# Kernel tuning notes

Measured on AMD Instinct MI355X. Metric: run time of the kernel, lower is better.

The kernel has to match this reference:

```python
import jax, jax.numpy as jnp
import numpy as np

N_STFT = 513
N_BARKS = 128
SAMPLE_RATE = 16000
F_MIN = 0.0
F_MAX = 8000.0
MAX_ITER = 30
TOL_LOSS = 1e-5
TOL_CHANGE = 1e-8
LR = 0.1
MOMENTUM = 0.9
BATCH = 4
TIME = 512


def _hz_to_bark(f):
    # traunmuller scale
    b = 26.81 * f / (1960.0 + f) - 0.53
    b = jnp.where(b < 2.0, b + 0.15 * (2.0 - b), b)
    b = jnp.where(b > 20.1, b + 0.22 * (b - 20.1), b)
    return b


def _bark_to_hz(b):
    b = jnp.where(b < 2.0, (b - 0.3) / 0.85, b)
    b = jnp.where(b > 20.1, (b + 4.422) / 1.22, b)
    return 1960.0 * (b + 0.53) / (26.28 - b)


def barkscale_fbanks():
    all_freqs = jnp.linspace(0.0, float(SAMPLE_RATE // 2), N_STFT)
    b_min = _hz_to_bark(jnp.float32(F_MIN))
    b_max = _hz_to_bark(jnp.float32(F_MAX))
    b_pts = jnp.linspace(b_min, b_max, N_BARKS + 2)
    f_pts = _bark_to_hz(b_pts)
    f_diff = f_pts[1:] - f_pts[:-1]                  # (n_barks+1,)
    slopes = f_pts[None, :] - all_freqs[:, None]     # (freq, n_barks+2)
    down = -slopes[:, :-2] / f_diff[:-1]
    up = slopes[:, 2:] / f_diff[1:]
    return jnp.maximum(0.0, jnp.minimum(down, up))   # (freq, n_barks)


def setup_inputs() -> dict:
    key = jax.random.key(0)
    k1, k2 = jax.random.split(key)
    barkspec = jax.random.uniform(k1, (BATCH, N_BARKS, TIME), dtype=jnp.float32)
    fb = barkscale_fbanks().astype(jnp.float32)                 # (freq, n_barks)
    spec_init = jax.random.uniform(k2, (BATCH, TIME, N_STFT), dtype=jnp.float32)
    return {"barkspec": barkspec, "fb": fb, "spec_init": spec_init}


def reference(barkspec, fb, spec_init):
    B, K, T = barkspec.shape
    m = jnp.swapaxes(barkspec, -1, -2)          # (B, T, n_barks)
    inv_n = 1.0 / (B * T)

    def step(carry, _):
        spec, buf, prev_loss, done = carry
        diff = m - jnp.einsum('btf,fk->btk', spec, fb)          # (B, T, K)
        loss = (diff * diff).sum(-1).mean()
        # closed-form grad of mean_{b,t} sum_k diff^2 wrt spec
        grad = (-2.0 * inv_n) * jnp.einsum('btk,fk->btf', diff, fb)
        # torch SGD with momentum, no dampening/nesterov
        buf_n = MOMENTUM * buf + grad
        spec_n = jnp.maximum(spec - LR * buf_n, 0.0)            # clamp(min=0)
        stop = (loss < TOL_LOSS) | (jnp.abs(prev_loss - loss) < TOL_CHANGE)
        spec = jnp.where(done, spec, spec_n)
        buf = jnp.where(done, buf, buf_n)
        prev = jnp.where(done, prev_loss, loss)
        return (spec, buf, prev, done | stop), None

    init = (spec_init, jnp.zeros_like(spec_init), jnp.float32(jnp.inf),
            jnp.array(False))
    (spec, _, _, _), _ = jax.lax.scan(step, init, None, length=MAX_ITER)
    return jnp.swapaxes(spec, -1, -2)           # (B, freq, T)
```

## Files before the change

### kernel.cpp

```cpp
#include <hip/hip_runtime.h>


#define NSTFT 513
#define NBARK 128
#define BATCH 4
#define TIME  512
#define MAXIT 30
#define NROWS (BATCH*TIME)
#define SA 6
#define SB 20

#define WS_L_OFF   16
#define WS_FT_OFF  256
#define WS_HA_OFF  8464
#define WS_HB_OFF  8976
#define WS_WT_OFF  9488
#define WS_BP_OFF  22848

__global__ __launch_bounds__(64) void setup_taps(const float* __restrict__ fb,
                                                 char* __restrict__ ws) {
    const int f = blockIdx.x, lane = threadIdx.x;
    const float2 v = ((const float2*)(fb + (size_t)f * NBARK))[lane];
    unsigned long long mx = __ballot(v.x > 0.f);
    unsigned long long my = __ballot(v.y > 0.f);
    int kx = mx ? 2 * (__ffsll(mx) - 1)     : 999;
    int ky = my ? 2 * (__ffsll(my) - 1) + 1 : 999;
    int k1 = min(kx, ky);
    float w1 = 0.f, w2 = 0.f;
    if (k1 < NBARK) {
        float sx = __shfl(v.x, k1 >> 1);
        float sy = __shfl(v.y, k1 >> 1);
        w1 = (k1 & 1) ? sy : sx;
        const int k2 = k1 + 1;
        if (k2 < NBARK) {
            float tx = __shfl(v.x, k2 >> 1);
            float ty = __shfl(v.y, k2 >> 1);
            w2 = (k2 & 1) ? ty : tx;
        }
    } else {
        k1 = (f < 256) ? 0 : 127;
    }
    if (lane == 0) {
        float4 e;
        e.x = __int_as_float(k1); e.y = w1;
        e.z = 0.f;                e.w = w2;
        ((float4*)(ws + WS_FT_OFF))[f] = e;
    }
}

__global__ __launch_bounds__(64) void setup_lanes(char* __restrict__ ws) {
    const int c = blockIdx.x, lane = threadIdx.x;
    const float4* ftab = (const float4*)(ws + WS_FT_OFF);
    int fmin = 0x7fffffff, fmax = -1;
#pragma unroll
    for (int s = 0; s < 9; ++s) {
        int f = lane + 64*s;
        if (f < NSTFT) {
            float4 e = ftab[f];
            if (__float_as_int(e.x) == c) { fmin = min(fmin, f); fmax = max(fmax, f); }
        }
    }
#pragma unroll
    for (int m = 32; m; m >>= 1) {
        fmin = min(fmin, __shfl_xor(fmin, m));
        fmax = max(fmax, __shfl_xor(fmax, m));
    }
    int cnt = (fmax >= 0) ? (fmax - fmin + 1) : 0;
    if (fmax < 0) fmin = 0;
    const int cap  = (c < 64) ? SA : SB;
    const int base = (c < 64) ? 0  : SA;
    const int lf   = (c < 64) ? c  : 127 - c;
    cnt = min(cnt, cap);
    if (lane == 0)
        ((int2*)(ws + (c < 64 ? WS_HA_OFF : WS_HB_OFF)))[lf] =
            make_int2(fmin, cnt);
    if (lane < cap) {
        float2 wv = make_float2(0.f, 0.f);
        if (lane < cnt) {
            float4 e = ftab[fmin + lane];
            wv = make_float2(e.y, e.w);
        }
        ((float2*)(ws + WS_WT_OFF))[(base + lane)*64 + lf] = wv;
    }
}

__global__ __launch_bounds__(64, 2) void
iter_kernel(const float* __restrict__ barkspec,
            const float* __restrict__ spec_init,
            float* __restrict__ out,
            char* __restrict__ ws, int mode)
{
    const int lane = threadIdx.x;

    int niter = MAXIT;
    if (mode) {
        const float* losses = (const float*)(ws + WS_L_OFF);
        float prev = __builtin_inff();
        int S = MAXIT;
        for (int i = 0; i < MAXIT; ++i) {
            float l = losses[i];
            if (l < 1e-5f || fabsf(prev - l) < 1e-8f) { S = i + 1; break; }
            prev = l;
        }
        if (S >= MAXIT) return;
        niter = S;
    }

    const int r     = blockIdx.x;
    const int batch = r >> 9;
    const int t     = r & (TIME - 1);

    const int2 hA = ((const int2*)(ws + WS_HA_OFF))[lane];
    const int2 hB = ((const int2*)(ws + WS_HB_OFF))[lane];
    const float2* wt = (const float2*)(ws + WS_WT_OFF);
    const float* spg = spec_init + ((size_t)batch*TIME + t)*NSTFT;

    float w1A[SA], w2A[SA], spA[SA], bfA[SA];
    float w1B[SB], w2B[SB], spB[SB], bfB[SB];
#pragma unroll
    for (int i = 0; i < SA; ++i) {
        float2 v = wt[i*64 + lane];
        w1A[i] = v.x; w2A[i] = v.y;
        spA[i] = (i < hA.y) ? spg[hA.x + i] : 0.f;
        bfA[i] = 0.f;
    }
#pragma unroll
    for (int i = 0; i < SB; ++i) {
        float2 v = wt[(SA + i)*64 + lane];
        w1B[i] = v.x; w2B[i] = v.y;
        spB[i] = (i < hB.y) ? spg[hB.x + i] : 0.f;
        bfB[i] = 0.f;
    }

    const float* bs = barkspec + (size_t)batch*NBARK*TIME + t;
    const float m0 = bs[(size_t)lane*TIME];
    const float m1 = bs[(size_t)(127 - lane)*TIME];

    float* bpL = (float*)(ws + WS_BP_OFF) + (size_t)r*64 + lane;
    const float GC = -2.0f / (float)NROWS;

    for (int it = 0; it < niter; ++it) {
        float sBA = 0.f, sBB0 = 0.f, sBB1 = 0.f;
#pragma unroll
        for (int i = 0; i < SA; ++i) sBA = fmaf(spA[i], w2A[i], sBA);
#pragma unroll
        for (int i = 0; i < SB/2; ++i) sBB0 = fmaf(spB[i], w2B[i], sBB0);
#pragma unroll
        for (int i = SB/2; i < SB; ++i) sBB1 = fmaf(spB[i], w2B[i], sBB1);
        const float sBB = sBB0 + sBB1;
        float cAin = __shfl_up(sBA, 1);
        float cBin = __shfl_down(sBB, 1);

        float sAA = 0.f, sAB0 = 0.f, sAB1 = 0.f;
#pragma unroll
        for (int i = 0; i < SA; ++i) sAA = fmaf(spA[i], w1A[i], sAA);
#pragma unroll
        for (int i = 0; i < SB/2; ++i) sAB0 = fmaf(spB[i], w1B[i], sAB0);
#pragma unroll
        for (int i = SB/2; i < SB; ++i) sAB1 = fmaf(spB[i], w1B[i], sAB1);
        const float sAB = sAB0 + sAB1;

        if (lane == 0)  cAin = 0.f;
        if (lane == 63) cBin = sBA;
        const float d0 = m0 - (sAA + cAin);
        const float d1 = m1 - (sAB + cBin);

        if (!mode) { bpL[0] = fmaf(d0, d0, d1*d1); bpL += NROWS*64; }

        float dAn = __shfl_down(d0, 1);
        float dBn = __shfl_up(d1, 1);
        const float g0 = GC * d0, g1 = GC * d1;
#pragma unroll
        for (int i = 0; i < SA; ++i) bfA[i] *= 0.9f;
#pragma unroll
        for (int i = 0; i < SB; ++i) bfB[i] *= 0.9f;
        if (lane == 63) dAn = d1;
        const float gA = GC * dAn, gB = GC * dBn;
#pragma unroll
        for (int i = 0; i < SA; ++i) {
            float g = fmaf(g0, w1A[i], gA * w2A[i]);
            bfA[i] += g;
            float v = fmaf(-0.1f, bfA[i], spA[i]);
            spA[i] = v < 0.f ? 0.f : v;
        }
#pragma unroll
        for (int i = 0; i < SB; ++i) {
            float g = fmaf(g1, w1B[i], gB * w2B[i]);
            bfB[i] += g;
            float v = fmaf(-0.1f, bfB[i], spB[i]);
            spB[i] = v < 0.f ? 0.f : v;
        }
    }

    float* og = out + ((size_t)batch*NSTFT)*TIME + t;
#pragma unroll
    for (int i = 0; i < SA; ++i)
        if (i < hA.y) og[(size_t)(hA.x + i)*TIME] = spA[i];
#pragma unroll
    for (int i = 0; i < SB; ++i)
        if (i < hB.y) og[(size_t)(hB.x + i)*TIME] = spB[i];
}

__global__ __launch_bounds__(1024) void scan_reduce(char* __restrict__ ws) {
    __shared__ float wsum[16];
    const int it = blockIdx.x, tid = threadIdx.x;
    const int wave = tid >> 6, lane = tid & 63;
    const float4* b4 = (const float4*)((const float*)(ws + WS_BP_OFF)
                                       + (size_t)it*NROWS*64);
    float s = 0.f;
#pragma unroll
    for (int j = 0; j < 32; ++j) {
        float4 v = b4[tid + j*1024];
        s += (v.x + v.y) + (v.z + v.w);
    }
#pragma unroll
    for (int m = 32; m; m >>= 1) s += __shfl_xor(s, m);
    if (lane == 0) wsum[wave] = s;
    __syncthreads();
    if (wave == 0) {
        float v = (lane < 16) ? wsum[lane] : 0.f;
#pragma unroll
        for (int m = 8; m; m >>= 1) v += __shfl_xor(v, m);
        if (lane == 0)
            ((float*)(ws + WS_L_OFF))[it] = v * (1.0f/(float)NROWS);
    }
}

extern "C" void kernel_launch(void* const* d_in, const int* in_sizes, int n_in,
                              void* d_out, int out_size, void* d_ws, size_t ws_size,
                              hipStream_t stream)
{
    const float* barkspec  = (const float*)d_in[0];
    const float* fb        = (const float*)d_in[1];
    const float* spec_init = (const float*)d_in[2];
    float* out = (float*)d_out;
    char* ws = (char*)d_ws;

    setup_taps <<<NSTFT, 64, 0, stream>>>(fb, ws);
    setup_lanes<<<NBARK, 64, 0, stream>>>(ws);
    iter_kernel<<<NROWS, 64, 0, stream>>>(barkspec, spec_init, out, ws, 0);
    scan_reduce<<<MAXIT, 1024, 0, stream>>>(ws);
    iter_kernel<<<NROWS, 64, 0, stream>>>(barkspec, spec_init, out, ws, 1);
}
```

Measured before the change: 109.3 us.

## Process two time rows per wavefront and restructure shuffle dependency chain

Each 64-lane block now handles two adjacent time rows, sharing the per-lane filter weights in registers and halving the grid. The per-iteration schedule computes both dot products before any cross-lane shuffle, so all four shuffles run together and the d values are rebuilt algebraically. This is meant to give more independent work per wave to hide shuffle and FMA latency and to amortise weight loads. In exchange it doubles the state registers per thread, relaxes launch bounds to one block, and leaves fewer waves resident.

```diff
diff --git a/kernel.cpp b/kernel.cpp
--- a/kernel.cpp
+++ b/kernel.cpp
@@ -84,7 +84,7 @@
     }
 }
 
-__global__ __launch_bounds__(64, 2) void
+__global__ __launch_bounds__(64, 1) void
 iter_kernel(const float* __restrict__ barkspec,
             const float* __restrict__ spec_init,
             float* __restrict__ out,
@@ -106,99 +106,138 @@
         niter = S;
     }
 
-    const int r     = blockIdx.x;
-    const int batch = r >> 9;
-    const int t     = r & (TIME - 1);
+    const int r0    = blockIdx.x * 2;
+    const int batch = r0 >> 9;
+    const int t0    = r0 & (TIME - 1);
 
     const int2 hA = ((const int2*)(ws + WS_HA_OFF))[lane];
     const int2 hB = ((const int2*)(ws + WS_HB_OFF))[lane];
     const float2* wt = (const float2*)(ws + WS_WT_OFF);
-    const float* spg = spec_init + ((size_t)batch*TIME + t)*NSTFT;
-
-    float w1A[SA], w2A[SA], spA[SA], bfA[SA];
-    float w1B[SB], w2B[SB], spB[SB], bfB[SB];
+    const float* spg = spec_init + ((size_t)batch*TIME + t0)*NSTFT;
+
+    float w1A[SA], w2A[SA], w1B[SB], w2B[SB];
+    float spA[2][SA], bfA[2][SA], spB[2][SB], bfB[2][SB];
 #pragma unroll
     for (int i = 0; i < SA; ++i) {
         float2 v = wt[i*64 + lane];
         w1A[i] = v.x; w2A[i] = v.y;
-        spA[i] = (i < hA.y) ? spg[hA.x + i] : 0.f;
-        bfA[i] = 0.f;
+        spA[0][i] = (i < hA.y) ? spg[hA.x + i] : 0.f;
+        spA[1][i] = (i < hA.y) ? spg[NSTFT + hA.x + i] : 0.f;
+        bfA[0][i] = 0.f; bfA[1][i] = 0.f;
     }
 #pragma unroll
     for (int i = 0; i < SB; ++i) {
         float2 v = wt[(SA + i)*64 + lane];
         w1B[i] = v.x; w2B[i] = v.y;
-        spB[i] = (i < hB.y) ? spg[hB.x + i] : 0.f;
-        bfB[i] = 0.f;
-    }
-
-    const float* bs = barkspec + (size_t)batch*NBARK*TIME + t;
-    const float m0 = bs[(size_t)lane*TIME];
-    const float m1 = bs[(size_t)(127 - lane)*TIME];
-
-    float* bpL = (float*)(ws + WS_BP_OFF) + (size_t)r*64 + lane;
+        spB[0][i] = (i < hB.y) ? spg[hB.x + i] : 0.f;
+        spB[1][i] = (i < hB.y) ? spg[NSTFT + hB.x + i] : 0.f;
+        bfB[0][i] = 0.f; bfB[1][i] = 0.f;
+    }
+
+    const float* bs = barkspec + (size_t)batch*NBARK*TIME + t0;
+    const float m0[2] = { bs[(size_t)lane*TIME],
+                          bs[(size_t)lane*TIME + 1] };
+    const float m1[2] = { bs[(size_t)(127 - lane)*TIME],
+                          bs[(size_t)(127 - lane)*TIME + 1] };
+
+    float* bp = (float*)(ws + WS_BP_OFF) + (size_t)r0*64 + lane;
     const float GC = -2.0f / (float)NROWS;
 
     for (int it = 0; it < niter; ++it) {
-        float sBA = 0.f, sBB0 = 0.f, sBB1 = 0.f;
-#pragma unroll
-        for (int i = 0; i < SA; ++i) sBA = fmaf(spA[i], w2A[i], sBA);
-#pragma unroll
-        for (int i = 0; i < SB/2; ++i) sBB0 = fmaf(spB[i], w2B[i], sBB0);
-#pragma unroll
-        for (int i = SB/2; i < SB; ++i) sBB1 = fmaf(spB[i], w2B[i], sBB1);
-        const float sBB = sBB0 + sBB1;
-        float cAin = __shfl_up(sBA, 1);
-        float cBin = __shfl_down(sBB, 1);
-
-        float sAA = 0.f, sAB0 = 0.f, sAB1 = 0.f;
-#pragma unroll
-        for (int i = 0; i < SA; ++i) sAA = fmaf(spA[i], w1A[i], sAA);
-#pragma unroll
-        for (int i = 0; i < SB/2; ++i) sAB0 = fmaf(spB[i], w1B[i], sAB0);
-#pragma unroll
-        for (int i = SB/2; i < SB; ++i) sAB1 = fmaf(spB[i], w1B[i], sAB1);
-        const float sAB = sAB0 + sAB1;
-
-        if (lane == 0)  cAin = 0.f;
-        if (lane == 63) cBin = sBA;
-        const float d0 = m0 - (sAA + cAin);
-        const float d1 = m1 - (sAB + cBin);
-
-        if (!mode) { bpL[0] = fmaf(d0, d0, d1*d1); bpL += NROWS*64; }
-
-        float dAn = __shfl_down(d0, 1);
-        float dBn = __shfl_up(d1, 1);
-        const float g0 = GC * d0, g1 = GC * d1;
-#pragma unroll
-        for (int i = 0; i < SA; ++i) bfA[i] *= 0.9f;
-#pragma unroll
-        for (int i = 0; i < SB; ++i) bfB[i] *= 0.9f;
-        if (lane == 63) dAn = d1;
-        const float gA = GC * dAn, gB = GC * dBn;
-#pragma unroll
-        for (int i = 0; i < SA; ++i) {
-            float g = fmaf(g0, w1A[i], gA * w2A[i]);
-            bfA[i] += g;
-            float v = fmaf(-0.1f, bfA[i], spA[i]);
-            spA[i] = v < 0.f ? 0.f : v;
-        }
-#pragma unroll
-        for (int i = 0; i < SB; ++i) {
-            float g = fmaf(g1, w1B[i], gB * w2B[i]);
-            bfB[i] += g;
-            float v = fmaf(-0.1f, bfB[i], spB[i]);
-            spB[i] = v < 0.f ? 0.f : v;
-        }
-    }
-
-    float* og = out + ((size_t)batch*NSTFT)*TIME + t;
+        float d0[2], d1[2], dAn[2], dBn[2];
+        float sBA[2], sBB[2], u0[2], u1[2];
+#pragma unroll
+        for (int x = 0; x < 2; ++x) {
+            float a = 0.f, b0 = 0.f, b1 = 0.f, c = 0.f, e0 = 0.f, e1 = 0.f;
+#pragma unroll
+            for (int i = 0; i < SA; ++i) {
+                a = fmaf(spA[x][i], w2A[i], a);
+                c = fmaf(spA[x][i], w1A[i], c);
+            }
+#pragma unroll
+            for (int i = 0; i < SB/2; ++i) {
+                b0 = fmaf(spB[x][i], w2B[i], b0);
+                e0 = fmaf(spB[x][i], w1B[i], e0);
+            }
+#pragma unroll
+            for (int i = SB/2; i < SB; ++i) {
+                b1 = fmaf(spB[x][i], w2B[i], b1);
+                e1 = fmaf(spB[x][i], w1B[i], e1);
+            }
+            sBA[x] = a; sBB[x] = b0 + b1;
+            u0[x] = m0[x] - c; u1[x] = m1[x] - (e0 + e1);
+        }
+
+        float sa[2], sb[2], sp_[2], sq[2];
+#pragma unroll
+        for (int x = 0; x < 2; ++x) {
+            sa[x] = __shfl_up(sBA[x], 1);
+            sb[x] = __shfl_down(sBB[x], 1);
+            sp_[x] = __shfl_down(u0[x], 1);
+            sq[x] = __shfl_up(u1[x], 1);
+        }
+
+#pragma unroll
+        for (int x = 0; x < 2; ++x) {
+#pragma unroll
+            for (int i = 0; i < SA; ++i) bfA[x][i] *= 0.9f;
+#pragma unroll
+            for (int i = 0; i < SB; ++i) bfB[x][i] *= 0.9f;
+        }
+
+#pragma unroll
+        for (int x = 0; x < 2; ++x) {
+            float a = sa[x], b = sb[x];
+            if (lane == 0)  a = 0.f;
+            if (lane == 63) b = sBA[x];
+            d0[x] = u0[x] - a;
+            d1[x] = u1[x] - b;
+            float dn = sp_[x] - sBA[x];
+            if (lane == 63) dn = d1[x];
+            dAn[x] = dn;
+            dBn[x] = sq[x] - sBB[x];
+        }
+
+        if (!mode) {
+            bp[0]  = fmaf(d0[0], d0[0], d1[0]*d1[0]);
+            bp[64] = fmaf(d0[1], d0[1], d1[1]*d1[1]);
+            bp += NROWS*64;
+        }
+
+#pragma unroll
+        for (int x = 0; x < 2; ++x) {
+            const float g0 = GC * d0[x], g1 = GC * d1[x];
+            const float gA = GC * dAn[x], gB = GC * dBn[x];
+#pragma unroll
+            for (int i = 0; i < SA; ++i) {
+                float g = fmaf(g0, w1A[i], gA * w2A[i]);
+                bfA[x][i] += g;
+                float v = fmaf(-0.1f, bfA[x][i], spA[x][i]);
+                spA[x][i] = v < 0.f ? 0.f : v;
+            }
+#pragma unroll
+            for (int i = 0; i < SB; ++i) {
+                float g = fmaf(g1, w1B[i], gB * w2B[i]);
+                bfB[x][i] += g;
+                float v = fmaf(-0.1f, bfB[x][i], spB[x][i]);
+                spB[x][i] = v < 0.f ? 0.f : v;
+            }
+        }
+    }
+
+    float* og = out + ((size_t)batch*NSTFT)*TIME + t0;
 #pragma unroll
     for (int i = 0; i < SA; ++i)
-        if (i < hA.y) og[(size_t)(hA.x + i)*TIME] = spA[i];
+        if (i < hA.y) {
+            og[(size_t)(hA.x + i)*TIME]     = spA[0][i];
+            og[(size_t)(hA.x + i)*TIME + 1] = spA[1][i];
+        }
 #pragma unroll
     for (int i = 0; i < SB; ++i)
-        if (i < hB.y) og[(size_t)(hB.x + i)*TIME] = spB[i];
+        if (i < hB.y) {
+            og[(size_t)(hB.x + i)*TIME]     = spB[0][i];
+            og[(size_t)(hB.x + i)*TIME + 1] = spB[1][i];
+        }
 }
 
 __global__ __launch_bounds__(1024) void scan_reduce(char* __restrict__ ws) {
@@ -238,7 +277,7 @@
 
     setup_taps <<<NSTFT, 64, 0, stream>>>(fb, ws);
     setup_lanes<<<NBARK, 64, 0, stream>>>(ws);
-    iter_kernel<<<NROWS, 64, 0, stream>>>(barkspec, spec_init, out, ws, 0);
+    iter_kernel<<<NROWS/2, 64, 0, stream>>>(barkspec, spec_init, out, ws, 0);
     scan_reduce<<<MAXIT, 1024, 0, stream>>>(ws);
-    iter_kernel<<<NROWS, 64, 0, stream>>>(barkspec, spec_init, out, ws, 1);
-}
+    iter_kernel<<<NROWS/2, 64, 0, stream>>>(barkspec, spec_init, out, ws, 1);
+}
```

After: 108.5 us. Within noise of the previous version (-0.7%).
